# Kernel optimization log

Measured on AMD Instinct MI355X. Metric: run time of the kernel, lower is better.

The kernel has to match this reference:

```python
import jax, jax.numpy as jnp
import numpy as np

N_IN = 1_000_000   # active input voxels
N_OUT = 250_000    # active output voxels after stride-2 downsample
K = 8              # 2x2x2 kernel offsets
P = 125_000        # indice pairs per kernel offset (K*P == N_IN)
C_IN = 64
C_OUT = 128
EPS = 1e-5         # BatchNorm1d default eps


def setup_inputs() -> dict:
    key = jax.random.key(0)
    k0, k1, k2, k3 = jax.random.split(key, 4)
    features = jax.random.normal(k0, (N_IN, C_IN), jnp.float32)
    # per-offset gather/scatter index pairs (spconv indice_pairs)
    in_idx = jax.random.randint(k1, (K, P), 0, N_IN)
    out_idx = jax.random.randint(k2, (K, P), 0, N_OUT)
    # SubM/SparseConv weight: one [C_in, C_out] matrix per kernel offset
    weight = jax.random.normal(k3, (K, C_IN, C_OUT), jnp.float32) / np.sqrt(K * C_IN).astype(np.float32)
    gamma = jnp.ones((C_OUT,), jnp.float32)
    beta = jnp.zeros((C_OUT,), jnp.float32)
    return {"features": features, "weight": weight, "gamma": gamma,
            "beta": beta, "in_idx": in_idx, "out_idx": out_idx, "n_out": N_OUT}


def reference(features, weight, gamma, beta, in_idx, out_idx, n_out):
    # gather-GEMM-scatter sparse conv (no bias)
    gathered = features[in_idx]                              # [K, P, C_in]
    contrib = jnp.einsum('kpc,kcd->kpd', gathered, weight)   # [K, P, C_out]
    out = jnp.zeros((n_out, contrib.shape[-1]), features.dtype)
    out = out.at[out_idx.reshape(-1)].add(contrib.reshape(-1, contrib.shape[-1]))
    # BatchNorm1d (training mode: batch stats, biased variance) + ReLU
    mean = out.mean(axis=0)
    var = out.var(axis=0)
    y = (out - mean) * jax.lax.rsqrt(var + EPS) * gamma + beta
    return jax.nn.relu(y)
```

## Files before the change

kernel.cpp:

```cpp
#include <hip/hip_runtime.h>
#include <hip/hip_fp16.h>

#define N_IN   1000000
#define N_OUT  250000
#define KOFF   8
#define PPAIR  125000
#define C_IN   64
#define C_OUT  128
#define BN_EPS 1e-5f

typedef __attribute__((ext_vector_type(8))) short short8;
typedef __attribute__((ext_vector_type(4))) float floatx4;

__device__ __forceinline__ unsigned short f2bf(float x) {
    unsigned u = __float_as_uint(x);
    unsigned r = u + 0x7FFF + ((u >> 16) & 1);
    return (unsigned short)(r >> 16);
}

__global__ __launch_bounds__(256) void pack_w(
    const float* __restrict__ W, unsigned short* __restrict__ wp)
{
    int e = blockIdx.x * 256 + threadIdx.x;
    int k = e >> 13;
    int rem = e & 8191;
    int i = rem >> 7;
    int n = rem & 127;
    wp[k * 8192 + n * 64 + i] = f2bf(W[e]);
}

template <bool PK>
__global__ __launch_bounds__(256) void scatter_mfma(
    const float*          __restrict__ feat,
    const unsigned short* __restrict__ wpack,
    const int*            __restrict__ in_idx,
    const int*            __restrict__ out_idx,
    __half*               __restrict__ hacc,
    float*                __restrict__ facc)
{
    const int lane = threadIdx.x & 63;
    const int wave = threadIdx.x >> 6;
    const int quad = lane >> 4;
    const int col  = lane & 15;
    const int k    = blockIdx.y;
    const int base = blockIdx.x * 64 + wave * 16;

    const int gp_a = base + col;
    const int iid  = (gp_a < PPAIR) ? in_idx[k * PPAIR + gp_a] : 0;
    const float* frow = feat + (long)iid * C_IN;

    short8 afrag[2];
#pragma unroll
    for (int s = 0; s < 2; ++s) {
        const float4 f0 = *(const float4*)(frow + s * 32 + quad * 8);
        const float4 f1 = *(const float4*)(frow + s * 32 + quad * 8 + 4);
        short8 a;
        a[0] = (short)f2bf(f0.x); a[1] = (short)f2bf(f0.y);
        a[2] = (short)f2bf(f0.z); a[3] = (short)f2bf(f0.w);
        a[4] = (short)f2bf(f1.x); a[5] = (short)f2bf(f1.y);
        a[6] = (short)f2bf(f1.z); a[7] = (short)f2bf(f1.w);
        afrag[s] = a;
    }

    const unsigned short* wk = wpack + k * 8192;
    short8 bfrag[2][8];
#pragma unroll
    for (int s = 0; s < 2; ++s)
#pragma unroll
        for (int t = 0; t < 8; ++t)
            bfrag[s][t] = *(const short8*)(wk + (t * 16 + col) * 64 + s * 32 + quad * 8);

    floatx4 acc[8];
#pragma unroll
    for (int t = 0; t < 8; ++t) acc[t] = (floatx4){0.f, 0.f, 0.f, 0.f};
#pragma unroll
    for (int s = 0; s < 2; ++s)
#pragma unroll
        for (int t = 0; t < 8; ++t)
            acc[t] = __builtin_amdgcn_mfma_f32_16x16x32_bf16(
                afrag[s], bfrag[s][t], acc[t], 0, 0, 0);

    int oid[4];
#pragma unroll
    for (int r = 0; r < 4; ++r) {
        const int gp = base + quad * 4 + r;
        oid[r] = (gp < PPAIR) ? out_idx[k * PPAIR + gp] : -1;
    }

    if (PK) {
#pragma unroll
        for (int t = 0; t < 8; ++t)
#pragma unroll
            for (int r = 0; r < 4; ++r) {
                const float v = acc[t][r];
                const float w = __shfl_xor(v, 1, 64);
                if (oid[r] >= 0 && !(lane & 1)) {
                    const __half2 h = __halves2half2(__float2half(v), __float2half(w));
                    unsafeAtomicAdd((__half2*)(hacc + (long)oid[r] * C_OUT + t * 16 + col), h);
                }
            }
    } else {
#pragma unroll
        for (int t = 0; t < 8; ++t)
#pragma unroll
            for (int r = 0; r < 4; ++r)
                if (oid[r] >= 0)
                    atomicAdd(facc + (long)oid[r] * C_OUT + t * 16 + col, acc[t][r]);
    }
}

__global__ __launch_bounds__(256) void bn_stats_h(
    const __half* __restrict__ hacc, float* __restrict__ sums)
{
    const int c2 = threadIdx.x & 63;
    const int g  = threadIdx.x >> 6;
    float s0 = 0.f, s1 = 0.f, q0 = 0.f, q1 = 0.f;
    for (int r = blockIdx.x * 4 + g; r < N_OUT; r += gridDim.x * 4) {
        const __half2 h = ((const __half2*)hacc)[(long)r * 64 + c2];
        const float2 f = __half22float2(h);
        s0 += f.x; s1 += f.y;
        q0 = fmaf(f.x, f.x, q0); q1 = fmaf(f.y, f.y, q1);
    }
    __shared__ float4 ls[256];
    ls[threadIdx.x] = make_float4(s0, s1, q0, q1);
    __syncthreads();
    if (g == 0) {
        float4 a = ls[c2], b = ls[64 + c2], c = ls[128 + c2], d = ls[192 + c2];
        atomicAdd(&sums[2 * c2],       a.x + b.x + c.x + d.x);
        atomicAdd(&sums[2 * c2 + 1],   a.y + b.y + c.y + d.y);
        atomicAdd(&sums[128 + 2 * c2],     a.z + b.z + c.z + d.z);
        atomicAdd(&sums[128 + 2 * c2 + 1], a.w + b.w + c.w + d.w);
    }
}

__global__ __launch_bounds__(512) void bn_stats_f(
    const float* __restrict__ out, float* __restrict__ sums)
{
    const int c = threadIdx.x & 127;
    const int g = threadIdx.x >> 7;
    float s = 0.f, q = 0.f;
    for (int r = blockIdx.x * 4 + g; r < N_OUT; r += gridDim.x * 4) {
        const float x = out[(long)r * C_OUT + c];
        s += x; q = fmaf(x, x, q);
    }
    __shared__ float ls[512], lq[512];
    ls[threadIdx.x] = s; lq[threadIdx.x] = q;
    __syncthreads();
    if (g == 0) {
        atomicAdd(&sums[c],       ls[c] + ls[128 + c] + ls[256 + c] + ls[384 + c]);
        atomicAdd(&sums[128 + c], lq[c] + lq[128 + c] + lq[256 + c] + lq[384 + c]);
    }
}

__global__ __launch_bounds__(128) void bn_finalize(
    const float* __restrict__ sums,
    const float* __restrict__ gamma,
    const float* __restrict__ beta,
    float*       __restrict__ ss)
{
    const int c = threadIdx.x;
    const float inv_n = 1.0f / (float)N_OUT;
    const float mean  = sums[c] * inv_n;
    const float var   = sums[128 + c] * inv_n - mean * mean;
    const float sc    = gamma[c] * rsqrtf(var + BN_EPS);
    ss[c]       = sc;
    ss[128 + c] = fmaf(-mean, sc, beta[c]);
}

__global__ __launch_bounds__(256) void bn_apply_h(
    const __half* __restrict__ hacc,
    const float*  __restrict__ ss,
    float*        __restrict__ out)
{
    const long j = (long)blockIdx.x * 256 + threadIdx.x;
    const __half2 h0 = ((const __half2*)hacc)[j * 2];
    const __half2 h1 = ((const __half2*)hacc)[j * 2 + 1];
    const float2 f0 = __half22float2(h0);
    const float2 f1 = __half22float2(h1);
    const int c = ((int)j & 31) * 4;
    float4 v;
    v.x = fmaxf(0.f, fmaf(f0.x, ss[c + 0], ss[128 + c + 0]));
    v.y = fmaxf(0.f, fmaf(f0.y, ss[c + 1], ss[128 + c + 1]));
    v.z = fmaxf(0.f, fmaf(f1.x, ss[c + 2], ss[128 + c + 2]));
    v.w = fmaxf(0.f, fmaf(f1.y, ss[c + 3], ss[128 + c + 3]));
    ((float4*)out)[j] = v;
}

__global__ __launch_bounds__(256) void bn_apply_f(
    float* __restrict__ out, const float* __restrict__ ss)
{
    const long j = (long)blockIdx.x * 256 + threadIdx.x;
    const int c = ((int)j & 31) * 4;
    float4 v = ((const float4*)out)[j];
    v.x = fmaxf(0.f, fmaf(v.x, ss[c + 0], ss[128 + c + 0]));
    v.y = fmaxf(0.f, fmaf(v.y, ss[c + 1], ss[128 + c + 1]));
    v.z = fmaxf(0.f, fmaf(v.z, ss[c + 2], ss[128 + c + 2]));
    v.w = fmaxf(0.f, fmaf(v.w, ss[c + 3], ss[128 + c + 3]));
    ((float4*)out)[j] = v;
}

extern "C" void kernel_launch(void* const* d_in, const int* in_sizes, int n_in,
                              void* d_out, int out_size, void* d_ws, size_t ws_size,
                              hipStream_t stream)
{
    const float* feat    = (const float*)d_in[0];
    const float* weight  = (const float*)d_in[1];
    const float* gamma   = (const float*)d_in[2];
    const float* beta    = (const float*)d_in[3];
    const int*   in_idx  = (const int*)  d_in[4];
    const int*   out_idx = (const int*)  d_in[5];
    float* out = (float*)d_out;

    const size_t HACC_BYTES = (size_t)N_OUT * C_OUT * sizeof(__half);
    const size_t BIG_NEED   = HACC_BYTES + 1024 + 131072 + 1024;
    const bool   big        = ws_size >= BIG_NEED;

    char* wsb = (char*)d_ws;
    __half* hacc;
    float* sums;
    unsigned short* wpack;
    if (big) {
        hacc  = (__half*)wsb;
        sums  = (float*)(wsb + HACC_BYTES);
        wpack = (unsigned short*)(wsb + HACC_BYTES + 1024);
    } else {
        hacc  = nullptr;
        sums  = (float*)wsb;
        wpack = (unsigned short*)(wsb + 1024);
    }
    float* ss = sums + 256;
    ss = (float*)((char*)wpack + 131072);

    if (big) {
        hipMemsetAsync(hacc, 0, HACC_BYTES, stream);
    } else {
        hipMemsetAsync(out, 0, (size_t)N_OUT * C_OUT * sizeof(float), stream);
    }
    hipMemsetAsync(sums, 0, 256 * sizeof(float), stream);

    pack_w<<<256, 256, 0, stream>>>(weight, wpack);

    dim3 g1((PPAIR + 63) / 64, KOFF);
    if (big)
        scatter_mfma<true><<<g1, 256, 0, stream>>>(feat, wpack, in_idx, out_idx, hacc, out);
    else
        scatter_mfma<false><<<g1, 256, 0, stream>>>(feat, wpack, in_idx, out_idx, hacc, out);

    if (big) bn_stats_h<<<256, 256, 0, stream>>>(hacc, sums);
    else     bn_stats_f<<<256, 512, 0, stream>>>(out, sums);

    bn_finalize<<<1, 128, 0, stream>>>(sums, gamma, beta, ss);

    const int nblk = (int)((long)N_OUT * C_OUT / 4 / 256);
    if (big) bn_apply_h<<<nblk, 256, 0, stream>>>(hacc, ss, out);
    else     bn_apply_f<<<nblk, 256, 0, stream>>>(out, ss);
}
```

Measured before the change: 840.8 us.

## Replace atomic scatter with counting-sort bucketed contributions and segmented reduce

Adds a counting sort over output indices (count, three-stage scan, cursor-based slot assignment) so the GEMM writes each fp16 contribution row to a private slot instead of issuing atomic adds. A segmented reduction kernel then sums each output row's contributions in fp32, writes the result, and accumulates the BatchNorm statistics in the same pass. This removes the atomic contention on the accumulator. In exchange it adds several small kernels, a 256 MB contribution buffer that is written and then re-read, and the path only runs when the workspace is large enough.

```diff
diff --git a/kernel.cpp b/kernel.cpp
--- a/kernel.cpp
+++ b/kernel.cpp
@@ -5,6 +5,7 @@
 #define N_OUT  250000
 #define KOFF   8
 #define PPAIR  125000
+#define NPAIR  1000000
 #define C_IN   64
 #define C_OUT  128
 #define BN_EPS 1e-5f
@@ -29,14 +30,70 @@
     wp[k * 8192 + n * 64 + i] = f2bf(W[e]);
 }
 
-template <bool PK>
+__global__ __launch_bounds__(256) void k_count(
+    const int* __restrict__ oidx, int* __restrict__ counts)
+{
+    int e = blockIdx.x * 256 + threadIdx.x;
+    if (e < NPAIR) atomicAdd(&counts[oidx[e]], 1);
+}
+
+__global__ __launch_bounds__(1024) void k_scanA(
+    const int* __restrict__ counts, int* __restrict__ rp, int* __restrict__ bsum)
+{
+    __shared__ int ls[1024];
+    const int tid = threadIdx.x;
+    const int i = blockIdx.x * 1024 + tid;
+    int v = (i < N_OUT) ? counts[i] : 0;
+    ls[tid] = v;
+    __syncthreads();
+    for (int d = 1; d < 1024; d <<= 1) {
+        int t = (tid >= d) ? ls[tid - d] : 0;
+        __syncthreads();
+        ls[tid] += t;
+        __syncthreads();
+    }
+    if (i < N_OUT) rp[i] = ls[tid] - v;
+    if (tid == 1023) bsum[blockIdx.x] = ls[1023];
+}
+
+__global__ __launch_bounds__(256) void k_scanB(int* __restrict__ bsum)
+{
+    __shared__ int ls[256];
+    const int tid = threadIdx.x;
+    int v = bsum[tid];
+    ls[tid] = v;
+    __syncthreads();
+    for (int d = 1; d < 256; d <<= 1) {
+        int t = (tid >= d) ? ls[tid - d] : 0;
+        __syncthreads();
+        ls[tid] += t;
+        __syncthreads();
+    }
+    bsum[tid] = ls[tid] - v;
+}
+
+__global__ __launch_bounds__(1024) void k_scanC(
+    int* __restrict__ rp, const int* __restrict__ bsum, int* __restrict__ cursor)
+{
+    const int i = blockIdx.x * 1024 + threadIdx.x;
+    if (i < N_OUT) {
+        int r = rp[i] + bsum[blockIdx.x];
+        rp[i] = r;
+        cursor[i] = r;
+    }
+    if (blockIdx.x == 0 && threadIdx.x == 0) rp[N_OUT] = NPAIR;
+}
+
+template <int MODE>
 __global__ __launch_bounds__(256) void scatter_mfma(
     const float*          __restrict__ feat,
     const unsigned short* __restrict__ wpack,
     const int*            __restrict__ in_idx,
     const int*            __restrict__ out_idx,
     __half*               __restrict__ hacc,
-    float*                __restrict__ facc)
+    float*                __restrict__ facc,
+    int*                  __restrict__ cursor,
+    __half*               __restrict__ contrib)
 {
     const int lane = threadIdx.x & 63;
     const int wave = threadIdx.x >> 6;
@@ -62,6 +119,15 @@
         afrag[s] = a;
     }
 
+    int myrank = 0;
+    if (MODE == 2) {
+        const int gp = base + lane;
+        if (lane < 16 && gp < PPAIR) {
+            const int o = out_idx[k * PPAIR + gp];
+            myrank = atomicAdd(&cursor[o], 1);
+        }
+    }
+
     const unsigned short* wk = wpack + k * 8192;
     short8 bfrag[2][8];
 #pragma unroll
@@ -80,32 +146,84 @@
             acc[t] = __builtin_amdgcn_mfma_f32_16x16x32_bf16(
                 afrag[s], bfrag[s][t], acc[t], 0, 0, 0);
 
-    int oid[4];
-#pragma unroll
-    for (int r = 0; r < 4; ++r) {
-        const int gp = base + quad * 4 + r;
-        oid[r] = (gp < PPAIR) ? out_idx[k * PPAIR + gp] : -1;
-    }
-
-    if (PK) {
-#pragma unroll
-        for (int t = 0; t < 8; ++t)
-#pragma unroll
-            for (int r = 0; r < 4; ++r) {
+    if (MODE == 2) {
+#pragma unroll
+        for (int r = 0; r < 4; ++r) {
+            const int row  = quad * 4 + r;
+            const int p    = __shfl(myrank, row);
+            const bool vld = (base + row) < PPAIR;
+#pragma unroll
+            for (int t = 0; t < 8; ++t) {
                 const float v = acc[t][r];
                 const float w = __shfl_xor(v, 1, 64);
-                if (oid[r] >= 0 && !(lane & 1)) {
+                if (vld && !(lane & 1)) {
                     const __half2 h = __halves2half2(__float2half(v), __float2half(w));
-                    unsafeAtomicAdd((__half2*)(hacc + (long)oid[r] * C_OUT + t * 16 + col), h);
+                    *reinterpret_cast<__half2*>(contrib + (long)p * C_OUT + t * 16 + col) = h;
                 }
             }
+        }
     } else {
-#pragma unroll
-        for (int t = 0; t < 8; ++t)
-#pragma unroll
-            for (int r = 0; r < 4; ++r)
-                if (oid[r] >= 0)
-                    atomicAdd(facc + (long)oid[r] * C_OUT + t * 16 + col, acc[t][r]);
+        int oid[4];
+#pragma unroll
+        for (int r = 0; r < 4; ++r) {
+            const int gp = base + quad * 4 + r;
+            oid[r] = (gp < PPAIR) ? out_idx[k * PPAIR + gp] : -1;
+        }
+        if (MODE == 1) {
+#pragma unroll
+            for (int t = 0; t < 8; ++t)
+#pragma unroll
+                for (int r = 0; r < 4; ++r) {
+                    const float v = acc[t][r];
+                    const float w = __shfl_xor(v, 1, 64);
+                    if (oid[r] >= 0 && !(lane & 1)) {
+                        const __half2 h = __halves2half2(__float2half(v), __float2half(w));
+                        unsafeAtomicAdd((__half2*)(hacc + (long)oid[r] * C_OUT + t * 16 + col), h);
+                    }
+                }
+        } else {
+#pragma unroll
+            for (int t = 0; t < 8; ++t)
+#pragma unroll
+                for (int r = 0; r < 4; ++r)
+                    if (oid[r] >= 0)
+                        atomicAdd(facc + (long)oid[r] * C_OUT + t * 16 + col, acc[t][r]);
+        }
+    }
+}
+
+__global__ __launch_bounds__(256) void k_reduce(
+    const __half* __restrict__ contrib,
+    const int*    __restrict__ rp,
+    float*        __restrict__ out,
+    float*        __restrict__ sums)
+{
+    const int lane = threadIdx.x & 63;
+    const int wv   = threadIdx.x >> 6;
+    const int gw   = blockIdx.x * 4 + wv;
+    const int NW   = gridDim.x * 4;
+    float s0 = 0.f, s1 = 0.f, q0 = 0.f, q1 = 0.f;
+    for (int r = gw; r < N_OUT; r += NW) {
+        const int b = rp[r], e = rp[r + 1];
+        float a0 = 0.f, a1 = 0.f;
+        for (int j = b; j < e; ++j) {
+            const __half2 h = ((const __half2*)contrib)[(long)j * 64 + lane];
+            const float2 f = __half22float2(h);
+            a0 += f.x; a1 += f.y;
+        }
+        ((float2*)out)[(long)r * 64 + lane] = make_float2(a0, a1);
+        s0 += a0; s1 += a1;
+        q0 = fmaf(a0, a0, q0); q1 = fmaf(a1, a1, q1);
+    }
+    __shared__ float4 ls[256];
+    ls[threadIdx.x] = make_float4(s0, s1, q0, q1);
+    __syncthreads();
+    if (wv == 0) {
+        float4 a = ls[lane], b = ls[64 + lane], c = ls[128 + lane], d = ls[192 + lane];
+        atomicAdd(&sums[2 * lane],           a.x + b.x + c.x + d.x);
+        atomicAdd(&sums[2 * lane + 1],       a.y + b.y + c.y + d.y);
+        atomicAdd(&sums[128 + 2 * lane],     a.z + b.z + c.z + d.z);
+        atomicAdd(&sums[128 + 2 * lane + 1], a.w + b.w + c.w + d.w);
     }
 }
 
@@ -126,8 +244,8 @@
     __syncthreads();
     if (g == 0) {
         float4 a = ls[c2], b = ls[64 + c2], c = ls[128 + c2], d = ls[192 + c2];
-        atomicAdd(&sums[2 * c2],       a.x + b.x + c.x + d.x);
-        atomicAdd(&sums[2 * c2 + 1],   a.y + b.y + c.y + d.y);
+        atomicAdd(&sums[2 * c2],           a.x + b.x + c.x + d.x);
+        atomicAdd(&sums[2 * c2 + 1],       a.y + b.y + c.y + d.y);
         atomicAdd(&sums[128 + 2 * c2],     a.z + b.z + c.z + d.z);
         atomicAdd(&sums[128 + 2 * c2 + 1], a.w + b.w + c.w + d.w);
     }
@@ -210,48 +328,73 @@
     const int*   in_idx  = (const int*)  d_in[4];
     const int*   out_idx = (const int*)  d_in[5];
     float* out = (float*)d_out;
+    char* wsb = (char*)d_ws;
+
+    const size_t CONTRIB_BYTES = (size_t)NPAIR * C_OUT * sizeof(__half);
+    const size_t OFF_RP   = CONTRIB_BYTES;
+    const size_t OFF_CUR  = OFF_RP   + 1048576;
+    const size_t OFF_CNT  = OFF_CUR  + 1048576;
+    const size_t OFF_BS   = OFF_CNT  + 1048576;
+    const size_t OFF_SUM  = OFF_BS   + 4096;
+    const size_t OFF_SS   = OFF_SUM  + 1024;
+    const size_t OFF_WP   = OFF_SS   + 1024;
+    const size_t NEED2    = OFF_WP + 131072;
 
     const size_t HACC_BYTES = (size_t)N_OUT * C_OUT * sizeof(__half);
-    const size_t BIG_NEED   = HACC_BYTES + 1024 + 131072 + 1024;
-    const bool   big        = ws_size >= BIG_NEED;
-
-    char* wsb = (char*)d_ws;
-    __half* hacc;
-    float* sums;
-    unsigned short* wpack;
-    if (big) {
-        hacc  = (__half*)wsb;
-        sums  = (float*)(wsb + HACC_BYTES);
-        wpack = (unsigned short*)(wsb + HACC_BYTES + 1024);
+    const size_t NEED1 = HACC_BYTES + 1024 + 1024 + 131072;
+
+    const int nblk_apply = (int)((long)N_OUT * C_OUT / 4 / 256);
+    dim3 g1((PPAIR + 63) / 64, KOFF);
+
+    if (ws_size >= NEED2) {
+        __half* contrib = (__half*)wsb;
+        int*    rp      = (int*)(wsb + OFF_RP);
+        int*    cursor  = (int*)(wsb + OFF_CUR);
+        int*    counts  = (int*)(wsb + OFF_CNT);
+        int*    bsum    = (int*)(wsb + OFF_BS);
+        float*  sums    = (float*)(wsb + OFF_SUM);
+        float*  ss      = (float*)(wsb + OFF_SS);
+        unsigned short* wpack = (unsigned short*)(wsb + OFF_WP);
+
+        hipMemsetAsync(counts, 0, (size_t)N_OUT * sizeof(int), stream);
+        hipMemsetAsync(sums, 0, 256 * sizeof(float), stream);
+
+        pack_w<<<256, 256, 0, stream>>>(weight, wpack);
+        k_count<<<(NPAIR + 255) / 256, 256, 0, stream>>>(out_idx, counts);
+        k_scanA<<<256, 1024, 0, stream>>>(counts, rp, bsum);
+        k_scanB<<<1, 256, 0, stream>>>(bsum);
+        k_scanC<<<256, 1024, 0, stream>>>(rp, bsum, cursor);
+        scatter_mfma<2><<<g1, 256, 0, stream>>>(feat, wpack, in_idx, out_idx,
+                                                nullptr, out, cursor, contrib);
+        k_reduce<<<2048, 256, 0, stream>>>(contrib, rp, out, sums);
+        bn_finalize<<<1, 128, 0, stream>>>(sums, gamma, beta, ss);
+        bn_apply_f<<<nblk_apply, 256, 0, stream>>>(out, ss);
+    } else if (ws_size >= NEED1) {
+        __half* hacc = (__half*)wsb;
+        float*  sums = (float*)(wsb + HACC_BYTES);
+        unsigned short* wpack = (unsigned short*)(wsb + HACC_BYTES + 1024);
+        float*  ss   = (float*)((char*)wpack + 131072);
+
+        hipMemsetAsync(hacc, 0, HACC_BYTES, stream);
+        hipMemsetAsync(sums, 0, 256 * sizeof(float), stream);
+        pack_w<<<256, 256, 0, stream>>>(weight, wpack);
+        scatter_mfma<1><<<g1, 256, 0, stream>>>(feat, wpack, in_idx, out_idx,
+                                                hacc, out, nullptr, nullptr);
+        bn_stats_h<<<256, 256, 0, stream>>>(hacc, sums);
+        bn_finalize<<<1, 128, 0, stream>>>(sums, gamma, beta, ss);
+        bn_apply_h<<<nblk_apply, 256, 0, stream>>>(hacc, ss, out);
     } else {
-        hacc  = nullptr;
-        sums  = (float*)wsb;
-        wpack = (unsigned short*)(wsb + 1024);
-    }
-    float* ss = sums + 256;
-    ss = (float*)((char*)wpack + 131072);
-
-    if (big) {
-        hipMemsetAsync(hacc, 0, HACC_BYTES, stream);
-    } else {
+        float* sums = (float*)wsb;
+        unsigned short* wpack = (unsigned short*)(wsb + 1024);
+        float* ss = (float*)(wsb + 1024 + 131072);
+
         hipMemsetAsync(out, 0, (size_t)N_OUT * C_OUT * sizeof(float), stream);
-    }
-    hipMemsetAsync(sums, 0, 256 * sizeof(float), stream);
-
-    pack_w<<<256, 256, 0, stream>>>(weight, wpack);
-
-    dim3 g1((PPAIR + 63) / 64, KOFF);
-    if (big)
-        scatter_mfma<true><<<g1, 256, 0, stream>>>(feat, wpack, in_idx, out_idx, hacc, out);
-    else
-        scatter_mfma<false><<<g1, 256, 0, stream>>>(feat, wpack, in_idx, out_idx, hacc, out);
-
-    if (big) bn_stats_h<<<256, 256, 0, stream>>>(hacc, sums);
-    else     bn_stats_f<<<256, 512, 0, stream>>>(out, sums);
-
-    bn_finalize<<<1, 128, 0, stream>>>(sums, gamma, beta, ss);
-
-    const int nblk = (int)((long)N_OUT * C_OUT / 4 / 256);
-    if (big) bn_apply_h<<<nblk, 256, 0, stream>>>(hacc, ss, out);
-    else     bn_apply_f<<<nblk, 256, 0, stream>>>(out, ss);
-}
+        hipMemsetAsync(sums, 0, 256 * sizeof(float), stream);
+        pack_w<<<256, 256, 0, stream>>>(weight, wpack);
+        scatter_mfma<0><<<g1, 256, 0, stream>>>(feat, wpack, in_idx, out_idx,
+                                                nullptr, out, nullptr, nullptr);
+        bn_stats_f<<<256, 512, 0, stream>>>(out, sums);
+        bn_finalize<<<1, 128, 0, stream>>>(sums, gamma, beta, ss);
+        bn_apply_f<<<nblk_apply, 256, 0, stream>>>(out, ss);
+    }
+}
```

After: 826.8 us. Within noise of the previous version (-1.7%).

## Bucket pairs by output tile and accumulate conv in shared memory with fused BN stats

Applied to the files above, without the earlier changes.

Replaces global fp16 atomic scatter with a counting sort of index pairs into buckets of 128 output rows per kernel offset (count, three-pass scan, fill). A per-tile kernel then runs the MFMA gather-GEMM for each bucket, accumulates results with LDS atomics into a 64KB tile, writes fp32 rows once and emits per-block BN partial sums, which removes the memset and stats pass over the fp16 buffer. It adds several small preprocessing kernels with global atomics. The large LDS tile limits occupancy, and blocks with uneven bucket sizes can leave the work unbalanced.

```diff
diff --git a/kernel.cpp b/kernel.cpp
--- a/kernel.cpp
+++ b/kernel.cpp
@@ -1,13 +1,16 @@
 #include <hip/hip_runtime.h>
-#include <hip/hip_fp16.h>
 
 #define N_IN   1000000
 #define N_OUT  250000
 #define KOFF   8
 #define PPAIR  125000
+#define NPAIR  1000000
 #define C_IN   64
 #define C_OUT  128
 #define BN_EPS 1e-5f
+#define NB     1954
+#define NBUK   16384
+#define PBLK   2048
 
 typedef __attribute__((ext_vector_type(8))) short short8;
 typedef __attribute__((ext_vector_type(4))) float floatx4;
@@ -29,13 +32,239 @@
     wp[k * 8192 + n * 64 + i] = f2bf(W[e]);
 }
 
-template <bool PK>
-__global__ __launch_bounds__(256) void scatter_mfma(
+__global__ __launch_bounds__(256) void k_count(
+    const int* __restrict__ oidx, int* __restrict__ counts)
+{
+    const int p = blockIdx.x * 256 + threadIdx.x;
+    const int k = blockIdx.y;
+    if (p < PPAIR) {
+        const int o = oidx[k * PPAIR + p];
+        atomicAdd(&counts[(o >> 7) * 8 + k], 1);
+    }
+}
+
+__global__ __launch_bounds__(1024) void k_scanA(
+    const int* __restrict__ counts, int* __restrict__ bp, int* __restrict__ bsum)
+{
+    __shared__ int ls[1024];
+    const int tid = threadIdx.x;
+    const int i = blockIdx.x * 1024 + tid;
+    int v = counts[i];
+    ls[tid] = v;
+    __syncthreads();
+    for (int d = 1; d < 1024; d <<= 1) {
+        int t = (tid >= d) ? ls[tid - d] : 0;
+        __syncthreads();
+        ls[tid] += t;
+        __syncthreads();
+    }
+    bp[i] = ls[tid] - v;
+    if (tid == 1023) bsum[blockIdx.x] = ls[1023];
+}
+
+__global__ __launch_bounds__(256) void k_scanB(int* __restrict__ bsum)
+{
+    __shared__ int ls[256];
+    const int tid = threadIdx.x;
+    int v = bsum[tid];
+    ls[tid] = v;
+    __syncthreads();
+    for (int d = 1; d < 256; d <<= 1) {
+        int t = (tid >= d) ? ls[tid - d] : 0;
+        __syncthreads();
+        ls[tid] += t;
+        __syncthreads();
+    }
+    bsum[tid] = ls[tid] - v;
+}
+
+__global__ __launch_bounds__(1024) void k_scanC(
+    int* __restrict__ bp, const int* __restrict__ bsum, int* __restrict__ cursor)
+{
+    const int i = blockIdx.x * 1024 + threadIdx.x;
+    const int r = bp[i] + bsum[blockIdx.x];
+    bp[i] = r;
+    cursor[i] = r;
+}
+
+__global__ __launch_bounds__(256) void k_fill(
+    const int* __restrict__ oidx, const int* __restrict__ iidx,
+    int* __restrict__ cursor, int* __restrict__ perm)
+{
+    const int p = blockIdx.x * 256 + threadIdx.x;
+    const int k = blockIdx.y;
+    if (p < PPAIR) {
+        const int o   = oidx[k * PPAIR + p];
+        const int iid = iidx[k * PPAIR + p];
+        const int slot = atomicAdd(&cursor[(o >> 7) * 8 + k], 1);
+        perm[slot] = iid | ((o & 127) << 20);
+    }
+}
+
+__global__ __launch_bounds__(256) void k_conv(
+    const float*          __restrict__ feat,
+    const unsigned short* __restrict__ wpack,
+    const int*            __restrict__ perm,
+    const int*            __restrict__ bp,
+    float*                __restrict__ out,
+    float*                __restrict__ part)
+{
+    __shared__ float lacc[16384];
+    const int tid  = threadIdx.x;
+    const int lane = tid & 63;
+    const int wave = tid >> 6;
+    const int quad = lane >> 4;
+    const int col  = lane & 15;
+    const int blk  = blockIdx.x;
+
+    {
+        const float4 z = make_float4(0.f, 0.f, 0.f, 0.f);
+#pragma unroll
+        for (int i = 0; i < 16; ++i)
+            ((float4*)lacc)[i * 256 + tid] = z;
+    }
+    __syncthreads();
+
+#pragma unroll
+    for (int kk = 0; kk < 2; ++kk) {
+        const int k = wave * 2 + kk;
+        const unsigned short* wk = wpack + k * 8192;
+        short8 bfrag[2][8];
+#pragma unroll
+        for (int s = 0; s < 2; ++s)
+#pragma unroll
+            for (int t = 0; t < 8; ++t)
+                bfrag[s][t] = *(const short8*)(wk + (t * 16 + col) * 64 + s * 32 + quad * 8);
+
+        const int b = blk * 8 + k;
+        const int start = bp[b], end = bp[b + 1];
+        for (int t0 = start; t0 < end; t0 += 16) {
+            const int j  = t0 + col;
+            const int jc = min(j, end - 1);
+            const int e2 = perm[jc];
+            const int iid      = e2 & 0xFFFFF;
+            const int orow_own = e2 >> 20;
+
+            const float* frow = feat + (long)iid * C_IN;
+            short8 afrag[2];
+#pragma unroll
+            for (int s = 0; s < 2; ++s) {
+                const float4 f0 = *(const float4*)(frow + s * 32 + quad * 8);
+                const float4 f1 = *(const float4*)(frow + s * 32 + quad * 8 + 4);
+                short8 a;
+                a[0] = (short)f2bf(f0.x); a[1] = (short)f2bf(f0.y);
+                a[2] = (short)f2bf(f0.z); a[3] = (short)f2bf(f0.w);
+                a[4] = (short)f2bf(f1.x); a[5] = (short)f2bf(f1.y);
+                a[6] = (short)f2bf(f1.z); a[7] = (short)f2bf(f1.w);
+                afrag[s] = a;
+            }
+
+            floatx4 acc[8];
+#pragma unroll
+            for (int t = 0; t < 8; ++t) acc[t] = (floatx4){0.f, 0.f, 0.f, 0.f};
+#pragma unroll
+            for (int s = 0; s < 2; ++s)
+#pragma unroll
+                for (int t = 0; t < 8; ++t)
+                    acc[t] = __builtin_amdgcn_mfma_f32_16x16x32_bf16(
+                        afrag[s], bfrag[s][t], acc[t], 0, 0, 0);
+
+#pragma unroll
+            for (int r = 0; r < 4; ++r) {
+                const int m = quad * 4 + r;
+                const int orow = __shfl(orow_own, m);
+                if (t0 + m < end) {
+                    const int flip = (orow & 1) << 4;
+#pragma unroll
+                    for (int t = 0; t < 8; ++t)
+                        atomicAdd(&lacc[orow * 128 + ((t * 16 + col) ^ flip)], acc[t][r]);
+                }
+            }
+        }
+    }
+    __syncthreads();
+
+    const int c = tid & 127;
+    const int h = tid >> 7;
+    float s = 0.f, q = 0.f;
+#pragma unroll 8
+    for (int r0 = 0; r0 < 64; ++r0) {
+        const int r = h * 64 + r0;
+        const float v = lacc[r * 128 + (c ^ ((r & 1) << 4))];
+        s += v; q = fmaf(v, v, q);
+    }
+
+    const long rowbase = (long)blk * 128;
+#pragma unroll
+    for (int it = 0; it < 16; ++it) {
+        const int row = it * 8 + (tid >> 5);
+        if (rowbase + row < N_OUT) {
+            const int c4 = (tid & 31) * 4;
+            const float4 v = *(const float4*)&lacc[row * 128 + (c4 ^ ((row & 1) << 4))];
+            *(float4*)&out[(rowbase + row) * 128 + c4] = v;
+        }
+    }
+
+    __syncthreads();
+    lacc[h * 128 + c]       = s;
+    lacc[256 + h * 128 + c] = q;
+    __syncthreads();
+    if (tid < 128) {
+        part[tid * PBLK + blk]         = lacc[tid] + lacc[128 + tid];
+        part[(128 + tid) * PBLK + blk] = lacc[256 + tid] + lacc[384 + tid];
+    }
+}
+
+__global__ __launch_bounds__(256) void bn_sumreduce(
+    const float* __restrict__ part, float* __restrict__ sums)
+{
+    const int c = blockIdx.x;
+    float s = 0.f;
+    for (int b = threadIdx.x; b < NB; b += 256)
+        s += part[c * PBLK + b];
+    __shared__ float ls[256];
+    ls[threadIdx.x] = s;
+    __syncthreads();
+    for (int d = 128; d > 0; d >>= 1) {
+        if (threadIdx.x < d) ls[threadIdx.x] += ls[threadIdx.x + d];
+        __syncthreads();
+    }
+    if (threadIdx.x == 0) sums[c] = ls[0];
+}
+
+__global__ __launch_bounds__(128) void bn_finalize(
+    const float* __restrict__ sums,
+    const float* __restrict__ gamma,
+    const float* __restrict__ beta,
+    float*       __restrict__ ss)
+{
+    const int c = threadIdx.x;
+    const float inv_n = 1.0f / (float)N_OUT;
+    const float mean  = sums[c] * inv_n;
+    const float var   = sums[128 + c] * inv_n - mean * mean;
+    const float sc    = gamma[c] * rsqrtf(var + BN_EPS);
+    ss[c]       = sc;
+    ss[128 + c] = fmaf(-mean, sc, beta[c]);
+}
+
+__global__ __launch_bounds__(256) void bn_apply_f(
+    float* __restrict__ out, const float* __restrict__ ss)
+{
+    const long j = (long)blockIdx.x * 256 + threadIdx.x;
+    const int c = ((int)j & 31) * 4;
+    float4 v = ((const float4*)out)[j];
+    v.x = fmaxf(0.f, fmaf(v.x, ss[c + 0], ss[128 + c + 0]));
+    v.y = fmaxf(0.f, fmaf(v.y, ss[c + 1], ss[128 + c + 1]));
+    v.z = fmaxf(0.f, fmaf(v.z, ss[c + 2], ss[128 + c + 2]));
+    v.w = fmaxf(0.f, fmaf(v.w, ss[c + 3], ss[128 + c + 3]));
+    ((float4*)out)[j] = v;
+}
+
+__global__ __launch_bounds__(256) void scatter_fp32(
     const float*          __restrict__ feat,
     const unsigned short* __restrict__ wpack,
     const int*            __restrict__ in_idx,
     const int*            __restrict__ out_idx,
-    __half*               __restrict__ hacc,
     float*                __restrict__ facc)
 {
     const int lane = threadIdx.x & 63;
@@ -86,51 +315,12 @@
         const int gp = base + quad * 4 + r;
         oid[r] = (gp < PPAIR) ? out_idx[k * PPAIR + gp] : -1;
     }
-
-    if (PK) {
-#pragma unroll
-        for (int t = 0; t < 8; ++t)
-#pragma unroll
-            for (int r = 0; r < 4; ++r) {
-                const float v = acc[t][r];
-                const float w = __shfl_xor(v, 1, 64);
-                if (oid[r] >= 0 && !(lane & 1)) {
-                    const __half2 h = __halves2half2(__float2half(v), __float2half(w));
-                    unsafeAtomicAdd((__half2*)(hacc + (long)oid[r] * C_OUT + t * 16 + col), h);
-                }
-            }
-    } else {
-#pragma unroll
-        for (int t = 0; t < 8; ++t)
-#pragma unroll
-            for (int r = 0; r < 4; ++r)
-                if (oid[r] >= 0)
-                    atomicAdd(facc + (long)oid[r] * C_OUT + t * 16 + col, acc[t][r]);
-    }
-}
-
-__global__ __launch_bounds__(256) void bn_stats_h(
-    const __half* __restrict__ hacc, float* __restrict__ sums)
-{
-    const int c2 = threadIdx.x & 63;
-    const int g  = threadIdx.x >> 6;
-    float s0 = 0.f, s1 = 0.f, q0 = 0.f, q1 = 0.f;
-    for (int r = blockIdx.x * 4 + g; r < N_OUT; r += gridDim.x * 4) {
-        const __half2 h = ((const __half2*)hacc)[(long)r * 64 + c2];
-        const float2 f = __half22float2(h);
-        s0 += f.x; s1 += f.y;
-        q0 = fmaf(f.x, f.x, q0); q1 = fmaf(f.y, f.y, q1);
-    }
-    __shared__ float4 ls[256];
-    ls[threadIdx.x] = make_float4(s0, s1, q0, q1);
-    __syncthreads();
-    if (g == 0) {
-        float4 a = ls[c2], b = ls[64 + c2], c = ls[128 + c2], d = ls[192 + c2];
-        atomicAdd(&sums[2 * c2],       a.x + b.x + c.x + d.x);
-        atomicAdd(&sums[2 * c2 + 1],   a.y + b.y + c.y + d.y);
-        atomicAdd(&sums[128 + 2 * c2],     a.z + b.z + c.z + d.z);
-        atomicAdd(&sums[128 + 2 * c2 + 1], a.w + b.w + c.w + d.w);
-    }
+#pragma unroll
+    for (int t = 0; t < 8; ++t)
+#pragma unroll
+        for (int r = 0; r < 4; ++r)
+            if (oid[r] >= 0)
+                atomicAdd(facc + (long)oid[r] * C_OUT + t * 16 + col, acc[t][r]);
 }
 
 __global__ __launch_bounds__(512) void bn_stats_f(
@@ -150,53 +340,6 @@
         atomicAdd(&sums[c],       ls[c] + ls[128 + c] + ls[256 + c] + ls[384 + c]);
         atomicAdd(&sums[128 + c], lq[c] + lq[128 + c] + lq[256 + c] + lq[384 + c]);
     }
-}
-
-__global__ __launch_bounds__(128) void bn_finalize(
-    const float* __restrict__ sums,
-    const float* __restrict__ gamma,
-    const float* __restrict__ beta,
-    float*       __restrict__ ss)
-{
-    const int c = threadIdx.x;
-    const float inv_n = 1.0f / (float)N_OUT;
-    const float mean  = sums[c] * inv_n;
-    const float var   = sums[128 + c] * inv_n - mean * mean;
-    const float sc    = gamma[c] * rsqrtf(var + BN_EPS);
-    ss[c]       = sc;
-    ss[128 + c] = fmaf(-mean, sc, beta[c]);
-}
-
-__global__ __launch_bounds__(256) void bn_apply_h(
-    const __half* __restrict__ hacc,
-    const float*  __restrict__ ss,
-    float*        __restrict__ out)
-{
-    const long j = (long)blockIdx.x * 256 + threadIdx.x;
-    const __half2 h0 = ((const __half2*)hacc)[j * 2];
-    const __half2 h1 = ((const __half2*)hacc)[j * 2 + 1];
-    const float2 f0 = __half22float2(h0);
-    const float2 f1 = __half22float2(h1);
-    const int c = ((int)j & 31) * 4;
-    float4 v;
-    v.x = fmaxf(0.f, fmaf(f0.x, ss[c + 0], ss[128 + c + 0]));
-    v.y = fmaxf(0.f, fmaf(f0.y, ss[c + 1], ss[128 + c + 1]));
-    v.z = fmaxf(0.f, fmaf(f1.x, ss[c + 2], ss[128 + c + 2]));
-    v.w = fmaxf(0.f, fmaf(f1.y, ss[c + 3], ss[128 + c + 3]));
-    ((float4*)out)[j] = v;
-}
-
-__global__ __launch_bounds__(256) void bn_apply_f(
-    float* __restrict__ out, const float* __restrict__ ss)
-{
-    const long j = (long)blockIdx.x * 256 + threadIdx.x;
-    const int c = ((int)j & 31) * 4;
-    float4 v = ((const float4*)out)[j];
-    v.x = fmaxf(0.f, fmaf(v.x, ss[c + 0], ss[128 + c + 0]));
-    v.y = fmaxf(0.f, fmaf(v.y, ss[c + 1], ss[128 + c + 1]));
-    v.z = fmaxf(0.f, fmaf(v.z, ss[c + 2], ss[128 + c + 2]));
-    v.w = fmaxf(0.f, fmaf(v.w, ss[c + 3], ss[128 + c + 3]));
-    ((float4*)out)[j] = v;
 }
 
 extern "C" void kernel_launch(void* const* d_in, const int* in_sizes, int n_in,
@@ -210,48 +353,58 @@
     const int*   in_idx  = (const int*)  d_in[4];
     const int*   out_idx = (const int*)  d_in[5];
     float* out = (float*)d_out;
-
-    const size_t HACC_BYTES = (size_t)N_OUT * C_OUT * sizeof(__half);
-    const size_t BIG_NEED   = HACC_BYTES + 1024 + 131072 + 1024;
-    const bool   big        = ws_size >= BIG_NEED;
-
     char* wsb = (char*)d_ws;
-    __half* hacc;
-    float* sums;
-    unsigned short* wpack;
-    if (big) {
-        hacc  = (__half*)wsb;
-        sums  = (float*)(wsb + HACC_BYTES);
-        wpack = (unsigned short*)(wsb + HACC_BYTES + 1024);
+
+    const size_t OFF_PERM = 0;
+    const size_t OFF_CNT  = 4194304;
+    const size_t OFF_BP   = OFF_CNT  + 65536;
+    const size_t OFF_CUR  = OFF_BP   + 65664;
+    const size_t OFF_BSUM = OFF_CUR  + 65536;
+    const size_t OFF_PART = OFF_BSUM + 1024;
+    const size_t OFF_SUM  = OFF_PART + (size_t)256 * PBLK * 4;
+    const size_t OFF_SS   = OFF_SUM  + 1024;
+    const size_t OFF_WP   = OFF_SS   + 1024;
+    const size_t NEED     = OFF_WP   + 131072;
+
+    const int nblk_apply = (int)((long)N_OUT * C_OUT / 4 / 256);
+
+    if (ws_size >= NEED) {
+        int*   perm   = (int*)(wsb + OFF_PERM);
+        int*   counts = (int*)(wsb + OFF_CNT);
+        int*   bp     = (int*)(wsb + OFF_BP);
+        int*   cursor = (int*)(wsb + OFF_CUR);
+        int*   bsum   = (int*)(wsb + OFF_BSUM);
+        float* part   = (float*)(wsb + OFF_PART);
+        float* sums   = (float*)(wsb + OFF_SUM);
+        float* ss     = (float*)(wsb + OFF_SS);
+        unsigned short* wpack = (unsigned short*)(wsb + OFF_WP);
+
+        hipMemsetAsync(counts, 0, NBUK * sizeof(int), stream);
+        hipMemsetAsync(bsum, 0, 1024, stream);
+
+        pack_w<<<256, 256, 0, stream>>>(weight, wpack);
+        dim3 gp2((PPAIR + 255) / 256, KOFF);
+        k_count<<<gp2, 256, 0, stream>>>(out_idx, counts);
+        k_scanA<<<16, 1024, 0, stream>>>(counts, bp, bsum);
+        k_scanB<<<1, 256, 0, stream>>>(bsum);
+        k_scanC<<<16, 1024, 0, stream>>>(bp, bsum, cursor);
+        k_fill<<<gp2, 256, 0, stream>>>(out_idx, in_idx, cursor, perm);
+        k_conv<<<NB, 256, 0, stream>>>(feat, wpack, perm, bp, out, part);
+        bn_sumreduce<<<256, 256, 0, stream>>>(part, sums);
+        bn_finalize<<<1, 128, 0, stream>>>(sums, gamma, beta, ss);
+        bn_apply_f<<<nblk_apply, 256, 0, stream>>>(out, ss);
     } else {
-        hacc  = nullptr;
-        sums  = (float*)wsb;
-        wpack = (unsigned short*)(wsb + 1024);
-    }
-    float* ss = sums + 256;
-    ss = (float*)((char*)wpack + 131072);
-
-    if (big) {
-        hipMemsetAsync(hacc, 0, HACC_BYTES, stream);
-    } else {
+        float* sums = (float*)wsb;
+        float* ss   = (float*)(wsb + 1024);
+        unsigned short* wpack = (unsigned short*)(wsb + 2048);
+
         hipMemsetAsync(out, 0, (size_t)N_OUT * C_OUT * sizeof(float), stream);
-    }
-    hipMemsetAsync(sums, 0, 256 * sizeof(float), stream);
-
-    pack_w<<<256, 256, 0, stream>>>(weight, wpack);
-
-    dim3 g1((PPAIR + 63) / 64, KOFF);
-    if (big)
-        scatter_mfma<true><<<g1, 256, 0, stream>>>(feat, wpack, in_idx, out_idx, hacc, out);
-    else
-        scatter_mfma<false><<<g1, 256, 0, stream>>>(feat, wpack, in_idx, out_idx, hacc, out);
-
-    if (big) bn_stats_h<<<256, 256, 0, stream>>>(hacc, sums);
-    else     bn_stats_f<<<256, 512, 0, stream>>>(out, sums);
-
-    bn_finalize<<<1, 128, 0, stream>>>(sums, gamma, beta, ss);
-
-    const int nblk = (int)((long)N_OUT * C_OUT / 4 / 256);
-    if (big) bn_apply_h<<<nblk, 256, 0, stream>>>(hacc, ss, out);
-    else     bn_apply_f<<<nblk, 256, 0, stream>>>(out, ss);
-}
+        hipMemsetAsync(sums, 0, 256 * sizeof(float), stream);
+        pack_w<<<256, 256, 0, stream>>>(weight, wpack);
+        dim3 g1((PPAIR + 63) / 64, KOFF);
+        scatter_fp32<<<g1, 256, 0, stream>>>(feat, wpack, in_idx, out_idx, out);
+        bn_stats_f<<<256, 512, 0, stream>>>(out, sums);
+        bn_finalize<<<1, 128, 0, stream>>>(sums, gamma, beta, ss);
+        bn_apply_f<<<nblk_apply, 256, 0, stream>>>(out, ss);
+    }
+}
```

Measured after the change: 1.128 ms. +34.2%, slower.
